# Performance work log

Hardware: AMD Instinct MI355X
Metric: run time of the kernel (lower is better)

## Reference

```python
import jax, jax.numpy as jnp
import numpy as np

CONF_THRES = 0.5   # self.conf_thres
NMS_THRES = 0.5    # self.nms_thres
PRE_NMS = 2048     # candidates kept before pairwise IoU
MAX_DET = 300      # padded detections returned per image
MAX_WH = 4096.0    # class-offset trick so NMS is per-class
IMG_SIZE = 416.0   # self.img_size; boxes_scale (416,416)->(416,416) => scale 1


def xywh2xyxy(b):
    xy, wh = b[..., :2], b[..., 2:4]
    return jnp.concatenate([xy - wh * 0.5, xy + wh * 0.5], axis=-1)


def pairwise_iou(boxes):
    # boxes: [K,4] xyxy -> [K,K] IoU
    area = (boxes[:, 2] - boxes[:, 0]) * (boxes[:, 3] - boxes[:, 1])
    lt = jnp.maximum(boxes[:, None, :2], boxes[None, :, :2])
    rb = jnp.minimum(boxes[:, None, 2:], boxes[None, :, 2:])
    wh = jnp.clip(rb - lt, 0.0)
    inter = wh[..., 0] * wh[..., 1]
    return inter / (area[:, None] + area[None, :] - inter + 1e-16)


def nms_single(pred):
    # pred: [N,85] = xywh(4) + objectness(1) + class scores(80)
    boxes = xywh2xyxy(pred[:, :4])
    obj = pred[:, 4]
    cls_scores = pred[:, 5:] * obj[:, None]        # conf = obj * class prob
    conf = jnp.max(cls_scores, axis=-1)
    cls_id = jnp.argmax(cls_scores, axis=-1)
    valid = obj >= CONF_THRES                      # confidence threshold filter
    score = jnp.where(valid, conf, -1.0)

    order = jnp.argsort(-score)[:PRE_NMS]          # sort desc, keep top PRE_NMS
    boxes_s = boxes[order]
    score_s = score[order]
    cls_s = cls_id[order]
    valid_s = valid[order]

    # per-class NMS via coordinate offset by class id
    off = cls_s.astype(boxes_s.dtype) * MAX_WH
    iou = pairwise_iou(boxes_s + off[:, None])     # [PRE_NMS, PRE_NMS]

    def body(keep, i):
        suppressed = jnp.any(keep & (iou[:, i] > NMS_THRES))
        k = valid_s[i] & ~suppressed
        return keep.at[i].set(k), k

    keep, _ = jax.lax.scan(body, jnp.zeros(PRE_NMS, dtype=bool), jnp.arange(PRE_NMS))

    final_score = jnp.where(keep, score_s, -1.0)
    top = jnp.argsort(-final_score)[:MAX_DET]
    kb, ks, kc, km = boxes_s[top], score_s[top], cls_s[top], keep[top]

    scale = IMG_SIZE / 416.0                       # boxes_scale (identity here)
    det = jnp.concatenate(
        [kb * scale, ks[:, None], kc[:, None].astype(kb.dtype)], axis=-1)
    return jnp.where(km[:, None], det, 0.0)        # [MAX_DET, 6] padded


def setup_inputs() -> dict:
    key = jax.random.key(0)
    predictions = jax.random.uniform(key, (16, 10647, 85), dtype=jnp.float32)
    return {"predictions": predictions}


def reference(predictions):
    # detections per image: [x1,y1,x2,y2,score,class], zero-padded to MAX_DET
    return jax.vmap(nms_single)(predictions)  # [B, MAX_DET, 6]
```

## Files before the change

### kernel.cpp

```cpp
#include <hip/hip_runtime.h>
#include <hip/hip_bf16.h>
#include <stdint.h>

typedef unsigned long long u64;
typedef unsigned int u32;
typedef unsigned short u16;

#define NANCH 10647
#define NBATCH 16
#define NSORT 16384
#define NSEL 2048
#define NWORD 32
#define NCLS 80
#define CONF_T 0.5f
#define NMS_T 0.5f
#define MAXDET 300
#define MAXWH 4096.0f
#define CANDCAP 10688
#define PART 1344

__global__ __launch_bounds__(1024) void k_zero(u32* __restrict__ p, int nwords) {
    for (int i = threadIdx.x; i < nwords; i += 1024) p[i] = 0;
}

__global__ __launch_bounds__(256) void k_prep(const float* __restrict__ pred,
                                              u64* __restrict__ keys,
                                              float4* __restrict__ boxes,
                                              int* __restrict__ cls,
                                              float* __restrict__ score,
                                              u32* __restrict__ ghist) {
    __shared__ float sm[128 * 85];
    __shared__ u32 ph[256];
    int b = blockIdx.y;
    int a0 = blockIdx.x * 128;
    int na = NANCH - a0; if (na > 128) na = 128;
    const float* src = pred + ((size_t)b * NANCH + a0) * 85;
    int tot = na * 85;
    ph[threadIdx.x] = 0;
    for (int i = threadIdx.x; i < tot; i += 256) sm[i] = src[i];
    __syncthreads();
    int t = threadIdx.x;
    u64 kk = 0;
    if (t < na) {
        const float* s = &sm[t * 85];
        float x = s[0], y = s[1], w = s[2], h = s[3], obj = s[4];
        float best = s[5] * obj; int arg = 0;
        #pragma unroll
        for (int c = 1; c < 80; ++c) {
            float v = s[5 + c] * obj;
            if (v > best) { best = v; arg = c; }
        }
        bool valid = obj >= CONF_T;
        float sc = valid ? best : -1.0f;
        int a = a0 + t;
        float4 bx;
        bx.x = x - w * 0.5f; bx.y = y - h * 0.5f;
        bx.z = x + w * 0.5f; bx.w = y + h * 0.5f;
        size_t o = (size_t)b * NANCH + a;
        boxes[o] = bx;
        cls[o] = arg;
        score[o] = sc;
        u32 u = __float_as_uint(sc);
        u32 v = (u & 0x80000000u) ? ~u : (u | 0x80000000u);
        u32 hi = ~v;
        kk = ((u64)hi << 32) | (u32)a;
        keys[(size_t)b * NSORT + a] = kk;
    }
    u32 bin = (t < na) ? (u32)(kk >> 56) : 0xFFFFFFFFu;
    int lane = t & 63;
    u64 rem = __ballot(t < na);
    while (rem) {
        int srcl = __ffsll((long long)rem) - 1;
        u32 lb = __shfl(bin, srcl);
        u64 same = __ballot(bin == lb) & rem;
        if (lane == srcl) atomicAdd(&ph[lb], (u32)__popcll(same));
        rem &= ~same;
    }
    __syncthreads();
    if (ph[threadIdx.x]) atomicAdd(&ghist[(size_t)b * 256 + threadIdx.x], ph[threadIdx.x]);
}

__global__ __launch_bounds__(1024) void k_scan(const u64* __restrict__ keys,
                                               const u32* __restrict__ ghist,
                                               u64* __restrict__ gsk,
                                               u64* __restrict__ gcand,
                                               u32* __restrict__ gcnt,
                                               u32* __restrict__ gcandcnt) {
    __shared__ u32 hist[256];
    __shared__ u32 hsc[256];
    __shared__ u32 s_D0;
    __shared__ u32 wcs[16], wcc[16];
    __shared__ u32 s_gbs, s_gbc;
    int b = blockIdx.y;
    int part = blockIdx.x;
    int tid = threadIdx.x;
    int lane = tid & 63, wv = tid >> 6;
    u64 below = (1ULL << lane) - 1ULL;
    const u64* KB = keys + (size_t)b * NSORT;

    if (tid < 256) hist[tid] = ghist[(size_t)b * 256 + tid];
    __syncthreads();
    if (tid < 64) {
        u32 h0 = hist[tid*4], h1 = hist[tid*4+1], h2 = hist[tid*4+2], h3 = hist[tid*4+3];
        u32 loc = h0 + h1 + h2 + h3;
        u32 p = loc;
        #pragma unroll
        for (int o = 1; o < 64; o <<= 1) { u32 t2 = __shfl_up(p, o); if (lane >= o) p += t2; }
        u32 base = p - loc;
        hsc[tid*4]   = base + h0;
        hsc[tid*4+1] = base + h0 + h1;
        hsc[tid*4+2] = base + h0 + h1 + h2;
        hsc[tid*4+3] = base + h0 + h1 + h2 + h3;
    }
    __syncthreads();
    if (tid < 256) {
        u32 inc = hsc[tid], cb = inc - hist[tid];
        if (cb < NSEL && NSEL <= inc) s_D0 = tid;
    }
    __syncthreads();
    u32 D0 = s_D0;

    u64 kk0 = 0, kk1 = 0;
    bool s0 = false, s1 = false, c0 = false, c1 = false;
    {
        int off = tid, i = part * PART + off;
        bool inb = (off < PART) && (i < NANCH);
        kk0 = inb ? KB[i] : 0ULL;
        u32 top = (u32)(kk0 >> 56);
        s0 = inb && (top < D0); c0 = inb && (top == D0);
    }
    {
        int off = 1024 + tid, i = part * PART + off;
        bool inb = (off < PART) && (i < NANCH);
        kk1 = inb ? KB[i] : 0ULL;
        u32 top = (u32)(kk1 >> 56);
        s1 = inb && (top < D0); c1 = inb && (top == D0);
    }
    u64 bs0 = __ballot(s0), bs1 = __ballot(s1);
    u64 bc0 = __ballot(c0), bc1 = __ballot(c1);
    if (lane == 0) {
        wcs[wv] = (u32)(__popcll(bs0) + __popcll(bs1));
        wcc[wv] = (u32)(__popcll(bc0) + __popcll(bc1));
    }
    __syncthreads();
    if (tid < 16) {
        u32 vs = wcs[tid], vc = wcc[tid];
        u32 ps = vs, pc = vc;
        #pragma unroll
        for (int o = 1; o < 16; o <<= 1) {
            u32 ts = __shfl_up(ps, o);
            u32 tc = __shfl_up(pc, o);
            if (tid >= o) { ps += ts; pc += tc; }
        }
        wcs[tid] = ps - vs;
        wcc[tid] = pc - vc;
        if (tid == 15) {
            s_gbs = ps ? atomicAdd(&gcnt[b], ps) : 0u;
            s_gbc = pc ? atomicAdd(&gcandcnt[b], pc) : 0u;
        }
    }
    __syncthreads();
    u64* SKB = gsk + (size_t)b * NSEL;
    u64* CDB = gcand + (size_t)b * CANDCAP;
    u32 base_s = s_gbs + wcs[wv];
    u32 base_c = s_gbc + wcc[wv];
    if (s0) SKB[base_s + __popcll(bs0 & below)] = kk0;
    if (s1) SKB[base_s + __popcll(bs0) + __popcll(bs1 & below)] = kk1;
    if (c0) CDB[base_c + __popcll(bc0 & below)] = kk0;
    if (c1) CDB[base_c + __popcll(bc0) + __popcll(bc1 & below)] = kk1;
}

__global__ __launch_bounds__(1024) void k_fin(const u64* __restrict__ gsk,
                                              const u64* __restrict__ gcand,
                                              const u32* __restrict__ gcnt,
                                              const u32* __restrict__ gcandcnt,
                                              const float4* __restrict__ boxes,
                                              const int* __restrict__ cls,
                                              const float* __restrict__ score,
                                              float4* __restrict__ sel_box,
                                              float4* __restrict__ sel_sbox,
                                              float* __restrict__ sel_area,
                                              float* __restrict__ sel_score,
                                              int* __restrict__ sel_cls) {
    __shared__ u64 sk[NSEL];
    __shared__ u64 cand[CANDCAP];
    __shared__ u32 hist[256];
    __shared__ u32 hsc[256];
    __shared__ u64 s_red[16];
    __shared__ u32 s_D, s_rank, s_cnt, s_cand;

    int b = blockIdx.x;
    int tid = threadIdx.x;
    int lane = tid & 63;
    u64 below = (1ULL << lane) - 1ULL;

    u32 skn = gcnt[b];
    u32 cn0 = gcandcnt[b];
    if (tid == 0) { s_cnt = skn; s_rank = NSEL - skn; s_cand = cn0; }
    for (int i = tid; i < NSEL; i += 1024)
        sk[i] = (i < (int)skn) ? gsk[(size_t)b * NSEL + i] : ~0ULL;
    for (u32 i = tid; i < cn0; i += 1024)
        cand[i] = gcand[(size_t)b * CANDCAP + i];
    __syncthreads();

    const int shifts2[5] = {48, 40, 32, 8, 0};
    for (int rr = 0; ; ++rr) {
        u32 cn = s_cand, r = s_rank;
        if (r == cn || rr == 5) {
            for (u32 i0 = 0; i0 < cn; i0 += 1024) {
                u32 i = i0 + tid;
                bool take = i < cn;
                u64 kk = take ? cand[i] : 0ULL;
                u64 bt = __ballot(take);
                u32 base = 0;
                if (lane == 0 && bt) base = atomicAdd(&s_cnt, (u32)__popcll(bt));
                base = __shfl(base, 0);
                if (take) sk[base + __popcll(bt & below)] = kk;
            }
            break;
        }
        if (r == 1) {
            u64 best = ~0ULL;
            for (u32 i = tid; i < cn; i += 1024) { u64 kk = cand[i]; if (kk < best) best = kk; }
            #pragma unroll
            for (int o = 32; o > 0; o >>= 1) {
                u64 other = __shfl_down(best, o);
                if (other < best) best = other;
            }
            if (lane == 0) s_red[tid >> 6] = best;
            __syncthreads();
            if (tid == 0) {
                u64 m = s_red[0];
                for (int w2 = 1; w2 < 16; ++w2) if (s_red[w2] < m) m = s_red[w2];
                sk[atomicAdd(&s_cnt, 1u)] = m;
            }
            break;
        }
        int shift = shifts2[rr];
        if (tid < 256) hist[tid] = 0;
        __syncthreads();
        for (u32 i = tid; i < cn; i += 1024)
            atomicAdd(&hist[(u32)(cand[i] >> shift) & 0xFFu], 1u);
        __syncthreads();
        if (tid < 64) {
            u32 h0 = hist[tid*4], h1 = hist[tid*4+1], h2 = hist[tid*4+2], h3 = hist[tid*4+3];
            u32 loc = h0 + h1 + h2 + h3;
            u32 p = loc;
            #pragma unroll
            for (int o = 1; o < 64; o <<= 1) { u32 t2 = __shfl_up(p, o); if (lane >= o) p += t2; }
            u32 base = p - loc;
            hsc[tid*4]   = base + h0;
            hsc[tid*4+1] = base + h0 + h1;
            hsc[tid*4+2] = base + h0 + h1 + h2;
            hsc[tid*4+3] = base + h0 + h1 + h2 + h3;
        }
        __syncthreads();
        if (tid < 256) {
            u32 inc = hsc[tid], cb = inc - hist[tid];
            if (cb < r && r <= inc) { s_D = tid; s_rank = r - cb; }
        }
        __syncthreads();
        u32 D = s_D;
        u64 vv[11]; bool vb[11];
        #pragma unroll
        for (int it = 0; it < 11; ++it) {
            u32 i = tid + it * 1024;
            vb[it] = (i < cn);
            vv[it] = vb[it] ? cand[i] : 0ULL;
        }
        __syncthreads();
        if (tid == 0) s_cand = 0;
        __syncthreads();
        #pragma unroll
        for (int it = 0; it < 11; ++it) {
            u32 dg = (u32)(vv[it] >> shift) & 0xFFu;
            bool tk = vb[it] && (dg < D);
            u64 bt = __ballot(tk);
            u32 base = 0;
            if (lane == 0 && bt) base = atomicAdd(&s_cnt, (u32)__popcll(bt));
            base = __shfl(base, 0);
            if (tk) sk[base + __popcll(bt & below)] = vv[it];
        }
        #pragma unroll
        for (int it = 0; it < 11; ++it) {
            u32 dg = (u32)(vv[it] >> shift) & 0xFFu;
            bool tk = vb[it] && (dg == D);
            u64 bt = __ballot(tk);
            u32 base = 0;
            if (lane == 0 && bt) base = atomicAdd(&s_cand, (u32)__popcll(bt));
            base = __shfl(base, 0);
            if (tk) cand[base + __popcll(bt & below)] = vv[it];
        }
        __syncthreads();
    }
    __syncthreads();

    {
        int w = tid >> 6, l = lane;
        int base = w * 128;
        u64 a = sk[base + l], c = sk[base + 64 + l];
        #pragma unroll
        for (int k = 2; k <= 128; k <<= 1) {
            for (int j = k >> 1; j > 0; j >>= 1) {
                if (j == 64) {
                    bool dir = (((base + l) & k) == 0);
                    u64 lo = a < c ? a : c;
                    u64 hi = a < c ? c : a;
                    a = dir ? lo : hi;
                    c = dir ? hi : lo;
                } else {
                    bool up_ = (l & j) != 0;
                    bool dira = (((base + l) & k) == 0);
                    bool dirc = (((base + 64 + l) & k) == 0);
                    u64 pa = __shfl_xor(a, j);
                    u64 pc = __shfl_xor(c, j);
                    a = (up_ == dira) ? (a > pa ? a : pa) : (a < pa ? a : pa);
                    c = (up_ == dirc) ? (c > pc ? c : pc) : (c < pc ? c : pc);
                }
            }
        }
        sk[base + l] = a; sk[base + 64 + l] = c;
        __syncthreads();
        for (int k = 256; k <= NSEL; k <<= 1) {
            for (int j = k >> 1; j >= 128; j >>= 1) {
                int n = tid;
                int i = ((n & ~(j - 1)) << 1) | (n & (j - 1));
                int l2 = i | j;
                u64 x = sk[i], y = sk[l2];
                bool up2 = ((i & k) == 0);
                if ((x > y) == up2) { sk[i] = y; sk[l2] = x; }
                __syncthreads();
            }
            a = sk[base + l]; c = sk[base + 64 + l];
            bool dirk = ((base & k) == 0);
            {
                u64 lo = a < c ? a : c;
                u64 hi = a < c ? c : a;
                a = dirk ? lo : hi;
                c = dirk ? hi : lo;
            }
            #pragma unroll
            for (int j = 32; j > 0; j >>= 1) {
                bool up_ = (l & j) != 0;
                u64 pa = __shfl_xor(a, j);
                u64 pc = __shfl_xor(c, j);
                a = (up_ == dirk) ? (a > pa ? a : pa) : (a < pa ? a : pa);
                c = (up_ == dirk) ? (c > pc ? c : pc) : (c < pc ? c : pc);
            }
            sk[base + l] = a; sk[base + 64 + l] = c;
            __syncthreads();
        }
    }

    for (int r2 = tid; r2 < NSEL; r2 += 1024) {
        u64 key = sk[r2];
        int a = (int)(key & 0xFFFFFFFFu);
        if ((unsigned)a >= NANCH) a = 0;
        size_t src = (size_t)b * NANCH + a;
        float4 bx = boxes[src];
        int c = cls[src];
        float sc = score[src];
        float off = (float)c * MAXWH;
        float4 sb;
        sb.x = bx.x + off; sb.y = bx.y + off;
        sb.z = bx.z + off; sb.w = bx.w + off;
        float area = (sb.z - sb.x) * (sb.w - sb.y);
        size_t o = (size_t)b * NSEL + r2;
        sel_box[o] = bx; sel_sbox[o] = sb; sel_area[o] = area;
        sel_score[o] = sc; sel_cls[o] = c;
    }
}

__global__ __launch_bounds__(1024) void k_cnms(const float4* __restrict__ sel_sbox,
                                               const float* __restrict__ sel_area,
                                               const int* __restrict__ sel_cls,
                                               const float* __restrict__ sel_score,
                                               u64* __restrict__ gkeep) {
    __shared__ u16 wmem[16][NSEL];
    __shared__ u64 wkeep[16][NWORD];

    int b = blockIdx.y;
    int cg = blockIdx.x;
    int lane = threadIdx.x & 63, wv = threadIdx.x >> 6;
    int c = cg * 16 + wv;
    size_t bb = (size_t)b * NSEL;
    const int* CL = sel_cls + bb;
    const float* SC = sel_score + bb;
    u64 below = (1ULL << lane) - 1ULL;

    int n = 0;
    for (int ch = 0; ch < NWORD; ++ch) {
        int i = ch * 64 + lane;
        bool pred = (CL[i] == c) && (SC[i] >= 0.0f);
        u64 bal = __ballot(pred);
        if (pred) wmem[wv][n + __popcll(bal & below)] = (u16)i;
        n += __popcll(bal);
    }

    for (int c0 = 0; c0 < n; c0 += 64) {
        int chunkn = n - c0; if (chunkn > 64) chunkn = 64;
        bool mv = lane < chunkn;
        int q = mv ? (int)wmem[wv][c0 + lane] : 0;
        float4 bq = sel_sbox[bb + q];
        float aq = sel_area[bb + q];

        bool hit = false;
        for (int j = 0; j < c0; ++j) {
            if (!((wkeep[wv][j >> 6] >> (j & 63)) & 1ULL)) continue;
            int p = (int)wmem[wv][j];
            float4 bp = sel_sbox[bb + p];
            float ap = sel_area[bb + p];
            float ltx = fmaxf(bp.x, bq.x), lty = fmaxf(bp.y, bq.y);
            float rbx = fminf(bp.z, bq.z), rby = fminf(bp.w, bq.w);
            float ww = fmaxf(rbx - ltx, 0.0f), hh = fmaxf(rby - lty, 0.0f);
            float inter = ww * hh;
            hit = hit || (mv && (inter / (ap + aq - inter + 1e-16f) > NMS_T));
        }
        u64 avail = __ballot(mv && !hit);

        u64 Rt = 0;
        for (int t = 0; t < chunkn; ++t) {
            int p = (int)wmem[wv][c0 + t];
            float4 bp = sel_sbox[bb + p];
            float ap = sel_area[bb + p];
            float ltx = fmaxf(bp.x, bq.x), lty = fmaxf(bp.y, bq.y);
            float rbx = fminf(bp.z, bq.z), rby = fminf(bp.w, bq.w);
            float ww = fmaxf(rbx - ltx, 0.0f), hh = fmaxf(rby - lty, 0.0f);
            float inter = ww * hh;
            u64 row = __ballot(mv && (inter / (ap + aq - inter + 1e-16f) > NMS_T));
            if (lane == t) Rt = row;
        }

        u64 U = avail, kept = 0;
        while (U) {
            bool inU = ((U >> lane) & 1ULL) != 0ULL;
            u64 newk = __ballot(inU && ((Rt & U & below) == 0ULL));
            u64 killed = __ballot((Rt & newk) != 0ULL);
            kept |= newk;
            U &= ~(newk | killed);
        }
        if (lane == 0) wkeep[wv][c0 >> 6] = kept;
        if ((kept >> lane) & 1ULL)
            atomicOr(&gkeep[(size_t)b * NWORD + (q >> 6)], 1ULL << (q & 63));
    }
}

__global__ __launch_bounds__(64) void k_out(const u64* __restrict__ gkeep,
                                            const float4* __restrict__ sel_box,
                                            const float* __restrict__ sel_score,
                                            const int* __restrict__ sel_cls,
                                            float* __restrict__ out) {
    int b = blockIdx.x;
    int lane = threadIdx.x;
    const float* SC = sel_score + (size_t)b * NSEL;
    u64 kreg = (lane < NWORD) ? gkeep[(size_t)b * NWORD + lane] : 0ULL;

    int cnt = (lane < NWORD) ? __popcll(kreg) : 0;
    int pre = cnt;
    #pragma unroll
    for (int dd = 1; dd < 64; dd <<= 1) {
        int o = __shfl_up(pre, dd);
        if (lane >= dd) pre += o;
    }
    int total = __shfl(pre, 63);
    int base = pre - cnt;
    float* OUT = out + (size_t)b * MAXDET * 6;
    if (lane < NWORD) {
        u64 m = kreg;
        int rr = 0;
        while (m) {
            int t = __ffsll((long long)m) - 1;
            m &= m - 1;
            int slot = base + rr; ++rr;
            if (slot < MAXDET) {
                int i = lane * 64 + t;
                size_t src = (size_t)b * NSEL + i;
                float4 bx = sel_box[src];
                float sc = SC[i];
                int c = sel_cls[src];
                float* o6 = OUT + slot * 6;
                o6[0] = bx.x; o6[1] = bx.y; o6[2] = bx.z; o6[3] = bx.w;
                o6[4] = sc; o6[5] = (float)c;
            }
        }
    }
    int start = total > MAXDET ? MAXDET : total;
    for (int s = start + lane; s < MAXDET; s += 64) {
        float* o6 = OUT + s * 6;
        o6[0] = 0.0f; o6[1] = 0.0f; o6[2] = 0.0f;
        o6[3] = 0.0f; o6[4] = 0.0f; o6[5] = 0.0f;
    }
}

extern "C" void kernel_launch(void* const* d_in, const int* in_sizes, int n_in,
                              void* d_out, int out_size, void* d_ws, size_t ws_size,
                              hipStream_t stream) {
    const float* pred = (const float*)d_in[0];
    float* out = (float*)d_out;

    char* ws = (char*)d_ws;
    size_t off = 0;
    auto alloc = [&](size_t bytes) -> void* {
        void* p = ws + off;
        off += (bytes + 255) & ~(size_t)255;
        return p;
    };

    u64*    keys      = (u64*)   alloc((size_t)NBATCH * NSORT * 8);
    float4* boxes     = (float4*)alloc((size_t)NBATCH * NANCH * 16);
    int*    cls       = (int*)   alloc((size_t)NBATCH * NANCH * 4);
    float*  score     = (float*) alloc((size_t)NBATCH * NANCH * 4);
    float4* sel_box   = (float4*)alloc((size_t)NBATCH * NSEL * 16);
    float4* sel_sbox  = (float4*)alloc((size_t)NBATCH * NSEL * 16);
    float*  sel_area  = (float*) alloc((size_t)NBATCH * NSEL * 4);
    float*  sel_score = (float*) alloc((size_t)NBATCH * NSEL * 4);
    int*    sel_cls   = (int*)   alloc((size_t)NBATCH * NSEL * 4);
    u64*    gsk       = (u64*)   alloc((size_t)NBATCH * NSEL * 8);
    u64*    gcand     = (u64*)   alloc((size_t)NBATCH * CANDCAP * 8);
    u64*    gkeep     = (u64*)   alloc((size_t)NBATCH * NWORD * 8);
    u32*    ghist     = (u32*)   alloc((size_t)NBATCH * 256 * 4);
    u32*    gcnt      = (u32*)   alloc((size_t)NBATCH * 4);
    u32*    gcandcnt  = (u32*)   alloc((size_t)NBATCH * 4);

    size_t zbytes = (char*)(gcandcnt + NBATCH) - (char*)gkeep;
    k_zero<<<1, 1024, 0, stream>>>((u32*)gkeep, (int)(zbytes / 4));

    dim3 g1((NANCH + 127) / 128, NBATCH);
    k_prep<<<g1, 256, 0, stream>>>(pred, keys, boxes, cls, score, ghist);

    dim3 g2(8, NBATCH);
    k_scan<<<g2, 1024, 0, stream>>>(keys, ghist, gsk, gcand, gcnt, gcandcnt);

    k_fin<<<NBATCH, 1024, 0, stream>>>(gsk, gcand, gcnt, gcandcnt,
                                       boxes, cls, score,
                                       sel_box, sel_sbox, sel_area,
                                       sel_score, sel_cls);

    dim3 g5(5, NBATCH);
    k_cnms<<<g5, 1024, 0, stream>>>(sel_sbox, sel_area, sel_cls, sel_score, gkeep);

    k_out<<<NBATCH, 64, 0, stream>>>(gkeep, sel_box, sel_score, sel_cls, out);
}
```

Measured before the change: 109.6 us.

## Fuse final select, per-class NMS and output into one per-image kernel

Merges k_fin, k_cnms and k_out into a single kernel per image that keeps the selected boxes, areas and classes in LDS, reusing the candidate buffer's space. It builds a compacted per-class index pool with a prefix sum, then runs the per-class greedy NMS from shared memory and writes the output directly. The score array is no longer stored; scores are decoded from the sort keys. This removes two launches and the global round trips of the selected arrays. In exchange, NMS runs on only 16 blocks (one per image) instead of 80, which cuts parallelism.

```diff
diff --git a/kernel.cpp b/kernel.cpp
--- a/kernel.cpp
+++ b/kernel.cpp
@@ -19,6 +19,12 @@
 #define CANDCAP 10688
 #define PART 1344
 
+__device__ __forceinline__ float dec_score(u64 key) {
+    u32 v = ~(u32)(key >> 32);
+    u32 u = (v & 0x80000000u) ? (v & 0x7FFFFFFFu) : ~v;
+    return __uint_as_float(u);
+}
+
 __global__ __launch_bounds__(1024) void k_zero(u32* __restrict__ p, int nwords) {
     for (int i = threadIdx.x; i < nwords; i += 1024) p[i] = 0;
 }
@@ -27,7 +33,6 @@
                                               u64* __restrict__ keys,
                                               float4* __restrict__ boxes,
                                               int* __restrict__ cls,
-                                              float* __restrict__ score,
                                               u32* __restrict__ ghist) {
     __shared__ float sm[128 * 85];
     __shared__ u32 ph[256];
@@ -59,7 +64,6 @@
         size_t o = (size_t)b * NANCH + a;
         boxes[o] = bx;
         cls[o] = arg;
-        score[o] = sc;
         u32 u = __float_as_uint(sc);
         u32 v = (u & 0x80000000u) ? ~u : (u | 0x80000000u);
         u32 hi = ~v;
@@ -170,28 +174,35 @@
     if (c1) CDB[base_c + __popcll(bc0) + __popcll(bc1 & below)] = kk1;
 }
 
-__global__ __launch_bounds__(1024) void k_fin(const u64* __restrict__ gsk,
-                                              const u64* __restrict__ gcand,
-                                              const u32* __restrict__ gcnt,
-                                              const u32* __restrict__ gcandcnt,
-                                              const float4* __restrict__ boxes,
-                                              const int* __restrict__ cls,
-                                              const float* __restrict__ score,
-                                              float4* __restrict__ sel_box,
-                                              float4* __restrict__ sel_sbox,
-                                              float* __restrict__ sel_area,
-                                              float* __restrict__ sel_score,
-                                              int* __restrict__ sel_cls) {
+__global__ __launch_bounds__(1024) void k_fused(const u64* __restrict__ gsk,
+                                                const u64* __restrict__ gcand,
+                                                const u32* __restrict__ gcnt,
+                                                const u32* __restrict__ gcandcnt,
+                                                const float4* __restrict__ boxes,
+                                                const int* __restrict__ cls,
+                                                float* __restrict__ out) {
     __shared__ u64 sk[NSEL];
-    __shared__ u64 cand[CANDCAP];
+    __shared__ __align__(16) char regA[CANDCAP*8];
+    __shared__ u16 pool[NSEL];
+    __shared__ u64 wk[16][NWORD];
+    __shared__ u32 skeep2[64];
+    __shared__ u64 vword[NWORD];
+    __shared__ u32 cnt[NCLS];
+    __shared__ u32 cbase[NCLS];
     __shared__ u32 hist[256];
     __shared__ u32 hsc[256];
     __shared__ u64 s_red[16];
-    __shared__ u32 s_D, s_rank, s_cnt, s_cand;
+    __shared__ u32 s_D, s_rank, s_cnt, s_cand, s_total;
+
+    u64*    cand = (u64*)regA;
+    float4* sbox = (float4*)regA;
+    float4* rbox = (float4*)(regA + 32768);
+    float*  sar  = (float*)(regA + 65536);
+    u16*    scls = (u16*)(regA + 73728);
 
     int b = blockIdx.x;
     int tid = threadIdx.x;
-    int lane = tid & 63;
+    int lane = tid & 63, wv = tid >> 6;
     u64 below = (1ULL << lane) - 1ULL;
 
     u32 skn = gcnt[b];
@@ -351,141 +362,161 @@
             __syncthreads();
         }
     }
-
-    for (int r2 = tid; r2 < NSEL; r2 += 1024) {
-        u64 key = sk[r2];
-        int a = (int)(key & 0xFFFFFFFFu);
-        if ((unsigned)a >= NANCH) a = 0;
-        size_t src = (size_t)b * NANCH + a;
-        float4 bx = boxes[src];
-        int c = cls[src];
-        float sc = score[src];
-        float off = (float)c * MAXWH;
-        float4 sb;
-        sb.x = bx.x + off; sb.y = bx.y + off;
-        sb.z = bx.z + off; sb.w = bx.w + off;
-        float area = (sb.z - sb.x) * (sb.w - sb.y);
-        size_t o = (size_t)b * NSEL + r2;
-        sel_box[o] = bx; sel_sbox[o] = sb; sel_area[o] = area;
-        sel_score[o] = sc; sel_cls[o] = c;
-    }
-}
-
-__global__ __launch_bounds__(1024) void k_cnms(const float4* __restrict__ sel_sbox,
-                                               const float* __restrict__ sel_area,
-                                               const int* __restrict__ sel_cls,
-                                               const float* __restrict__ sel_score,
-                                               u64* __restrict__ gkeep) {
-    __shared__ u16 wmem[16][NSEL];
-    __shared__ u64 wkeep[16][NWORD];
-
-    int b = blockIdx.y;
-    int cg = blockIdx.x;
-    int lane = threadIdx.x & 63, wv = threadIdx.x >> 6;
-    int c = cg * 16 + wv;
-    size_t bb = (size_t)b * NSEL;
-    const int* CL = sel_cls + bb;
-    const float* SC = sel_score + bb;
-    u64 below = (1ULL << lane) - 1ULL;
-
-    int n = 0;
-    for (int ch = 0; ch < NWORD; ++ch) {
-        int i = ch * 64 + lane;
-        bool pred = (CL[i] == c) && (SC[i] >= 0.0f);
-        u64 bal = __ballot(pred);
-        if (pred) wmem[wv][n + __popcll(bal & below)] = (u16)i;
-        n += __popcll(bal);
-    }
-
-    for (int c0 = 0; c0 < n; c0 += 64) {
-        int chunkn = n - c0; if (chunkn > 64) chunkn = 64;
-        bool mv = lane < chunkn;
-        int q = mv ? (int)wmem[wv][c0 + lane] : 0;
-        float4 bq = sel_sbox[bb + q];
-        float aq = sel_area[bb + q];
-
-        bool hit = false;
-        for (int j = 0; j < c0; ++j) {
-            if (!((wkeep[wv][j >> 6] >> (j & 63)) & 1ULL)) continue;
-            int p = (int)wmem[wv][j];
-            float4 bp = sel_sbox[bb + p];
-            float ap = sel_area[bb + p];
-            float ltx = fmaxf(bp.x, bq.x), lty = fmaxf(bp.y, bq.y);
-            float rbx = fminf(bp.z, bq.z), rby = fminf(bp.w, bq.w);
-            float ww = fmaxf(rbx - ltx, 0.0f), hh = fmaxf(rby - lty, 0.0f);
-            float inter = ww * hh;
-            hit = hit || (mv && (inter / (ap + aq - inter + 1e-16f) > NMS_T));
-        }
-        u64 avail = __ballot(mv && !hit);
-
-        u64 Rt = 0;
-        for (int t = 0; t < chunkn; ++t) {
-            int p = (int)wmem[wv][c0 + t];
-            float4 bp = sel_sbox[bb + p];
-            float ap = sel_area[bb + p];
-            float ltx = fmaxf(bp.x, bq.x), lty = fmaxf(bp.y, bq.y);
-            float rbx = fminf(bp.z, bq.z), rby = fminf(bp.w, bq.w);
-            float ww = fmaxf(rbx - ltx, 0.0f), hh = fmaxf(rby - lty, 0.0f);
-            float inter = ww * hh;
-            u64 row = __ballot(mv && (inter / (ap + aq - inter + 1e-16f) > NMS_T));
-            if (lane == t) Rt = row;
-        }
-
-        u64 U = avail, kept = 0;
-        while (U) {
-            bool inU = ((U >> lane) & 1ULL) != 0ULL;
-            u64 newk = __ballot(inU && ((Rt & U & below) == 0ULL));
-            u64 killed = __ballot((Rt & newk) != 0ULL);
-            kept |= newk;
-            U &= ~(newk | killed);
-        }
-        if (lane == 0) wkeep[wv][c0 >> 6] = kept;
-        if ((kept >> lane) & 1ULL)
-            atomicOr(&gkeep[(size_t)b * NWORD + (q >> 6)], 1ULL << (q & 63));
-    }
-}
-
-__global__ __launch_bounds__(64) void k_out(const u64* __restrict__ gkeep,
-                                            const float4* __restrict__ sel_box,
-                                            const float* __restrict__ sel_score,
-                                            const int* __restrict__ sel_cls,
-                                            float* __restrict__ out) {
-    int b = blockIdx.x;
-    int lane = threadIdx.x;
-    const float* SC = sel_score + (size_t)b * NSEL;
-    u64 kreg = (lane < NWORD) ? gkeep[(size_t)b * NWORD + lane] : 0ULL;
-
-    int cnt = (lane < NWORD) ? __popcll(kreg) : 0;
-    int pre = cnt;
+    __syncthreads();
+
+    {
+        #pragma unroll
+        for (int e = 0; e < 2; ++e) {
+            int r2 = tid + e * 1024;
+            u64 key = sk[r2];
+            int a = (int)(key & 0xFFFFFFFFu);
+            if ((unsigned)a >= NANCH) a = 0;
+            size_t src = (size_t)b * NANCH + a;
+            float4 bx = boxes[src];
+            int c = cls[src];
+            float off = (float)c * MAXWH;
+            float4 sb;
+            sb.x = bx.x + off; sb.y = bx.y + off;
+            sb.z = bx.z + off; sb.w = bx.w + off;
+            rbox[r2] = bx;
+            sbox[r2] = sb;
+            sar[r2] = (sb.z - sb.x) * (sb.w - sb.y);
+            scls[r2] = (u16)c;
+            u64 bv = __ballot((key >> 63) == 0ULL);
+            if (lane == 0) vword[wv + e * 16] = bv;
+        }
+    }
+    if (tid < 64) skeep2[tid] = 0;
+    __syncthreads();
+
     #pragma unroll
-    for (int dd = 1; dd < 64; dd <<= 1) {
-        int o = __shfl_up(pre, dd);
-        if (lane >= dd) pre += o;
-    }
-    int total = __shfl(pre, 63);
-    int base = pre - cnt;
+    for (int k5 = 0; k5 < 5; ++k5) {
+        int c = wv + 16 * k5;
+        int n = 0;
+        for (int ch = 0; ch < NWORD; ++ch) {
+            int i = ch * 64 + lane;
+            bool pred = (scls[i] == (u16)c) && (((vword[ch] >> lane) & 1ULL) != 0ULL);
+            u64 bal = __ballot(pred);
+            n += __popcll(bal);
+        }
+        if (lane == 0) cnt[c] = (u32)n;
+    }
+    __syncthreads();
+    if (wv == 0) {
+        u32 a0 = (lane < 40) ? cnt[2*lane] : 0;
+        u32 a1 = (lane < 40) ? cnt[2*lane+1] : 0;
+        u32 s = a0 + a1;
+        u32 p = s;
+        #pragma unroll
+        for (int o = 1; o < 64; o <<= 1) { u32 t2 = __shfl_up(p, o); if (lane >= o) p += t2; }
+        if (lane < 40) { cbase[2*lane] = p - s; cbase[2*lane+1] = p - s + a0; }
+    }
+    __syncthreads();
+    #pragma unroll
+    for (int k5 = 0; k5 < 5; ++k5) {
+        int c = wv + 16 * k5;
+        u32 run = cbase[c];
+        for (int ch = 0; ch < NWORD; ++ch) {
+            int i = ch * 64 + lane;
+            bool pred = (scls[i] == (u16)c) && (((vword[ch] >> lane) & 1ULL) != 0ULL);
+            u64 bal = __ballot(pred);
+            if (pred) pool[run + __popcll(bal & below)] = (u16)i;
+            run += (u32)__popcll(bal);
+        }
+    }
+    __syncthreads();
+
+    #pragma unroll
+    for (int k5 = 0; k5 < 5; ++k5) {
+        int c = wv + 16 * k5;
+        u32 nb = cbase[c];
+        int n = (int)cnt[c];
+        for (int c0 = 0; c0 < n; c0 += 64) {
+            int chunkn = n - c0; if (chunkn > 64) chunkn = 64;
+            bool mv = lane < chunkn;
+            int q = mv ? (int)pool[nb + c0 + lane] : 0;
+            float4 bq = sbox[q];
+            float aq = sar[q];
+
+            bool hit = false;
+            for (int j = 0; j < c0; ++j) {
+                if (!((wk[wv][j >> 6] >> (j & 63)) & 1ULL)) continue;
+                int p = (int)pool[nb + j];
+                float4 bp = sbox[p];
+                float ap = sar[p];
+                float ltx = fmaxf(bp.x, bq.x), lty = fmaxf(bp.y, bq.y);
+                float rbx2 = fminf(bp.z, bq.z), rby = fminf(bp.w, bq.w);
+                float ww = fmaxf(rbx2 - ltx, 0.0f), hh = fmaxf(rby - lty, 0.0f);
+                float inter = ww * hh;
+                hit = hit || (mv && (inter / (ap + aq - inter + 1e-16f) > NMS_T));
+            }
+            u64 avail = __ballot(mv && !hit);
+
+            u64 Rt = 0;
+            for (int t = 0; t < chunkn; ++t) {
+                int p = (int)pool[nb + c0 + t];
+                float4 bp = sbox[p];
+                float ap = sar[p];
+                float ltx = fmaxf(bp.x, bq.x), lty = fmaxf(bp.y, bq.y);
+                float rbx2 = fminf(bp.z, bq.z), rby = fminf(bp.w, bq.w);
+                float ww = fmaxf(rbx2 - ltx, 0.0f), hh = fmaxf(rby - lty, 0.0f);
+                float inter = ww * hh;
+                u64 row = __ballot(mv && (inter / (ap + aq - inter + 1e-16f) > NMS_T));
+                if (lane == t) Rt = row;
+            }
+
+            u64 U = avail, kept = 0;
+            while (U) {
+                bool inU = ((U >> lane) & 1ULL) != 0ULL;
+                u64 newk = __ballot(inU && ((Rt & U & below) == 0ULL));
+                u64 killed = __ballot((Rt & newk) != 0ULL);
+                kept |= newk;
+                U &= ~(newk | killed);
+            }
+            if (lane == 0) wk[wv][c0 >> 6] = kept;
+            if ((kept >> lane) & 1ULL)
+                atomicOr(&skeep2[q >> 5], 1u << (q & 31));
+        }
+    }
+    __syncthreads();
+
+    if (wv == 0) {
+        u64 kreg = (lane < NWORD)
+            ? (((u64)skeep2[2*lane+1] << 32) | (u64)skeep2[2*lane]) : 0ULL;
+        int cnt2 = __popcll(kreg);
+        int pre = cnt2;
+        #pragma unroll
+        for (int dd = 1; dd < 64; dd <<= 1) {
+            int o = __shfl_up(pre, dd);
+            if (lane >= dd) pre += o;
+        }
+        int total = __shfl(pre, 63);
+        int base = pre - cnt2;
+        float* OUT = out + (size_t)b * MAXDET * 6;
+        if (lane < NWORD) {
+            u64 m = kreg;
+            int rr = 0;
+            while (m) {
+                int t = __ffsll((long long)m) - 1;
+                m &= m - 1;
+                int slot = base + rr; ++rr;
+                if (slot < MAXDET) {
+                    int i = lane * 64 + t;
+                    float4 bx = rbox[i];
+                    float sc = dec_score(sk[i]);
+                    int c = (int)scls[i];
+                    float* o6 = OUT + slot * 6;
+                    o6[0] = bx.x; o6[1] = bx.y; o6[2] = bx.z; o6[3] = bx.w;
+                    o6[4] = sc; o6[5] = (float)c;
+                }
+            }
+        }
+        if (lane == 0) s_total = (total > MAXDET) ? (u32)MAXDET : (u32)total;
+    }
+    __syncthreads();
+    int start = (int)s_total;
     float* OUT = out + (size_t)b * MAXDET * 6;
-    if (lane < NWORD) {
-        u64 m = kreg;
-        int rr = 0;
-        while (m) {
-            int t = __ffsll((long long)m) - 1;
-            m &= m - 1;
-            int slot = base + rr; ++rr;
-            if (slot < MAXDET) {
-                int i = lane * 64 + t;
-                size_t src = (size_t)b * NSEL + i;
-                float4 bx = sel_box[src];
-                float sc = SC[i];
-                int c = sel_cls[src];
-                float* o6 = OUT + slot * 6;
-                o6[0] = bx.x; o6[1] = bx.y; o6[2] = bx.z; o6[3] = bx.w;
-                o6[4] = sc; o6[5] = (float)c;
-            }
-        }
-    }
-    int start = total > MAXDET ? MAXDET : total;
-    for (int s = start + lane; s < MAXDET; s += 64) {
+    for (int s = start + tid; s < MAXDET; s += 1024) {
         float* o6 = OUT + s * 6;
         o6[0] = 0.0f; o6[1] = 0.0f; o6[2] = 0.0f;
         o6[3] = 0.0f; o6[4] = 0.0f; o6[5] = 0.0f;
@@ -509,35 +540,21 @@
     u64*    keys      = (u64*)   alloc((size_t)NBATCH * NSORT * 8);
     float4* boxes     = (float4*)alloc((size_t)NBATCH * NANCH * 16);
     int*    cls       = (int*)   alloc((size_t)NBATCH * NANCH * 4);
-    float*  score     = (float*) alloc((size_t)NBATCH * NANCH * 4);
-    float4* sel_box   = (float4*)alloc((size_t)NBATCH * NSEL * 16);
-    float4* sel_sbox  = (float4*)alloc((size_t)NBATCH * NSEL * 16);
-    float*  sel_area  = (float*) alloc((size_t)NBATCH * NSEL * 4);
-    float*  sel_score = (float*) alloc((size_t)NBATCH * NSEL * 4);
-    int*    sel_cls   = (int*)   alloc((size_t)NBATCH * NSEL * 4);
     u64*    gsk       = (u64*)   alloc((size_t)NBATCH * NSEL * 8);
     u64*    gcand     = (u64*)   alloc((size_t)NBATCH * CANDCAP * 8);
-    u64*    gkeep     = (u64*)   alloc((size_t)NBATCH * NWORD * 8);
     u32*    ghist     = (u32*)   alloc((size_t)NBATCH * 256 * 4);
     u32*    gcnt      = (u32*)   alloc((size_t)NBATCH * 4);
     u32*    gcandcnt  = (u32*)   alloc((size_t)NBATCH * 4);
 
-    size_t zbytes = (char*)(gcandcnt + NBATCH) - (char*)gkeep;
-    k_zero<<<1, 1024, 0, stream>>>((u32*)gkeep, (int)(zbytes / 4));
+    size_t zbytes = (char*)(gcandcnt + NBATCH) - (char*)ghist;
+    k_zero<<<1, 1024, 0, stream>>>(ghist, (int)(zbytes / 4));
 
     dim3 g1((NANCH + 127) / 128, NBATCH);
-    k_prep<<<g1, 256, 0, stream>>>(pred, keys, boxes, cls, score, ghist);
+    k_prep<<<g1, 256, 0, stream>>>(pred, keys, boxes, cls, ghist);
 
     dim3 g2(8, NBATCH);
     k_scan<<<g2, 1024, 0, stream>>>(keys, ghist, gsk, gcand, gcnt, gcandcnt);
 
-    k_fin<<<NBATCH, 1024, 0, stream>>>(gsk, gcand, gcnt, gcandcnt,
-                                       boxes, cls, score,
-                                       sel_box, sel_sbox, sel_area,
-                                       sel_score, sel_cls);
-
-    dim3 g5(5, NBATCH);
-    k_cnms<<<g5, 1024, 0, stream>>>(sel_sbox, sel_area, sel_cls, sel_score, gkeep);
-
-    k_out<<<NBATCH, 64, 0, stream>>>(gkeep, sel_box, sel_score, sel_cls, out);
+    k_fused<<<NBATCH, 1024, 0, stream>>>(gsk, gcand, gcnt, gcandcnt,
+                                         boxes, cls, out);
 }
```

Result: slower. 129.4 us (+18.1%).
